# Optimization experiments

Measured on AMD Instinct MI355X. Metric: run time of the kernel, lower is better.

## Reference

```python
import jax, jax.numpy as jnp
import numpy as np

N = 100000
E = 800000
D = 128
THETA = (0.5, 0.3, 0.2)
NEG_SLOPE = 0.01  # torch F.leaky_relu default


def setup_inputs() -> dict:
    key = jax.random.key(0)
    ks = jax.random.split(key, 16)
    inv = 1.0 / np.sqrt(D)
    return {
        "src": jax.random.randint(ks[0], (E,), 0, N),
        "dst": jax.random.randint(ks[1], (E,), 0, N),
        "x0": jax.random.normal(ks[2], (N, D), jnp.float32),
        "x": jax.random.normal(ks[3], (N, D), jnp.float32),
        "e": jax.random.normal(ks[4], (N, D), jnp.float32),
        "labels": jax.random.randint(ks[5], (N,), 0, 2),
        "nid": jax.random.randint(ks[6], (N // 2,), 0, N),
        "alpha": jnp.full((1,), 0.5, jnp.float32),
        "emb": jax.random.normal(ks[7], (3, D), jnp.float32).at[2].set(0.0),  # padding_idx=2
        "pred_w1": jax.random.normal(ks[8], (D, D), jnp.float32) * inv,
        "pred_b1": jnp.zeros((D,), jnp.float32),
        "pred_w2": jax.random.normal(ks[9], (2, D), jnp.float32) * inv,
        "pred_b2": jnp.zeros((2,), jnp.float32),
        "weights": jax.random.uniform(ks[10], (2 * D, D), jnp.float32, -inv, inv),
        "lin_w": jax.random.normal(ks[11], (D, 2 * D), jnp.float32) * inv,
        "lin_b": jnp.zeros((D,), jnp.float32),
    }


def reference(src, dst, x0, x, e, labels, nid, alpha, emb,
              pred_w1, pred_b1, pred_w2, pred_b2, weights, lin_w, lin_b):
    # Predictor: MLP -> 2 logits, prob of class 1
    h = jax.nn.relu(x @ pred_w1.T + pred_b1)
    logits = h @ pred_w2.T + pred_b2                     # [N, 2]
    prob = jax.nn.softmax(logits, axis=1)[:, 1]          # [N]

    # NodeLabelEmbedding: soft mix of rows 0 and 1
    x_node = (1.0 - prob)[:, None] * emb[0] + prob[:, None] * emb[1]
    x_ = x
    xk = x + alpha * x_node

    # degree norm from edge list (in-degrees at dst)
    degs = jax.ops.segment_sum(jnp.ones_like(dst, dtype=xk.dtype), dst, num_segments=N)
    dinv = jnp.clip(degs, 1.0, None) ** -0.5             # [N]
    dinv = dinv[:, None]

    def unn_laplacian(feat):
        # feat - D^-1/2 A D^-1/2 feat  (messages src -> dst)
        msg = jax.ops.segment_sum((feat * dinv)[src], dst, num_segments=N)
        return feat - msg * dinv

    hi = THETA[0] * xk
    for k in range(1, len(THETA)):
        xk = unn_laplacian(xk)
        hi = hi + THETA[k] * xk

    hi = jnp.concatenate([hi, x_], axis=1)               # [N, 2D]
    outputs = hi @ weights                               # [N, D]
    out = jnp.concatenate([e, outputs], axis=1)          # [N, 2D]
    out = jax.nn.leaky_relu(out @ lin_w.T + lin_b, NEG_SLOPE)
    return out + x0                                      # residual
```

## Files before the change

kernel.cpp:

```cpp
#include <hip/hip_runtime.h>

#define N_NODES 100000
#define N_EDGES 800000
#define D 128

typedef __attribute__((ext_vector_type(8))) short short8;
typedef __attribute__((ext_vector_type(4))) float f32x4;

__device__ inline unsigned short f2bf(float f) {
  unsigned u = __float_as_uint(f);
  unsigned r = (u + 0x7fffu + ((u >> 16) & 1u)) >> 16;
  return (unsigned short)r;
}
__device__ inline void bfma8(float* acc, const uint4 v, float d) {
  acc[0] = fmaf(__uint_as_float(v.x << 16), d, acc[0]);
  acc[1] = fmaf(__uint_as_float(v.x & 0xffff0000u), d, acc[1]);
  acc[2] = fmaf(__uint_as_float(v.y << 16), d, acc[2]);
  acc[3] = fmaf(__uint_as_float(v.y & 0xffff0000u), d, acc[3]);
  acc[4] = fmaf(__uint_as_float(v.z << 16), d, acc[4]);
  acc[5] = fmaf(__uint_as_float(v.z & 0xffff0000u), d, acc[5]);
  acc[6] = fmaf(__uint_as_float(v.w << 16), d, acc[6]);
  acc[7] = fmaf(__uint_as_float(v.w & 0xffff0000u), d, acc[7]);
}
__device__ inline void unpack8(float* o, const uint4 v) {
  o[0] = __uint_as_float(v.x << 16); o[1] = __uint_as_float(v.x & 0xffff0000u);
  o[2] = __uint_as_float(v.y << 16); o[3] = __uint_as_float(v.y & 0xffff0000u);
  o[4] = __uint_as_float(v.z << 16); o[5] = __uint_as_float(v.z & 0xffff0000u);
  o[6] = __uint_as_float(v.w << 16); o[7] = __uint_as_float(v.w & 0xffff0000u);
}
__device__ inline uint4 pack8(const float* v) {
  uint4 r;
  r.x = (unsigned)f2bf(v[0]) | ((unsigned)f2bf(v[1]) << 16);
  r.y = (unsigned)f2bf(v[2]) | ((unsigned)f2bf(v[3]) << 16);
  r.z = (unsigned)f2bf(v[4]) | ((unsigned)f2bf(v[5]) << 16);
  r.w = (unsigned)f2bf(v[6]) | ((unsigned)f2bf(v[7]) << 16);
  return r;
}

__global__ void k_deg(const int* __restrict__ dst, int* __restrict__ degs) {
  int e = blockIdx.x * 256 + threadIdx.x;
  if (e < N_EDGES) atomicAdd(&degs[dst[e]], 1);
}

__global__ void k_scan1(const int* __restrict__ degs, int* __restrict__ offs,
                        int* __restrict__ aux) {
  __shared__ int s[256];
  int tid = threadIdx.x;
  int i = blockIdx.x * 256 + tid;
  int v = (i < N_NODES) ? degs[i] : 0;
  int sum = v;
  s[tid] = sum; __syncthreads();
  for (int off = 1; off < 256; off <<= 1) {
    int t = (tid >= off) ? s[tid - off] : 0;
    __syncthreads();
    sum += t; s[tid] = sum;
    __syncthreads();
  }
  if (i < N_NODES) offs[i] = sum - v;
  if (tid == 255) aux[blockIdx.x] = sum;
}

__global__ void k_scan2(const int* __restrict__ aux, int* __restrict__ aux2, int nblk) {
  __shared__ int s[512];
  int tid = threadIdx.x;
  int v = (tid < nblk) ? aux[tid] : 0;
  int sum = v;
  s[tid] = sum; __syncthreads();
  for (int off = 1; off < 512; off <<= 1) {
    int t = (tid >= off) ? s[tid - off] : 0;
    __syncthreads();
    sum += t; s[tid] = sum;
    __syncthreads();
  }
  aux2[tid] = sum - v;
}

__global__ void k_scan3(int* __restrict__ offs, const int* __restrict__ aux2,
                        const int* __restrict__ degs, float* __restrict__ dinv) {
  int i = blockIdx.x * 256 + threadIdx.x;
  if (i < N_NODES) {
    offs[i] += aux2[blockIdx.x];
    dinv[i] = rsqrtf(fmaxf((float)degs[i], 1.0f));
  }
}

__global__ void k_fill(const int* __restrict__ src, const int* __restrict__ dst,
                       const int* __restrict__ offs, int* __restrict__ cursor,
                       int* __restrict__ csr) {
  int e = blockIdx.x * 256 + threadIdx.x;
  if (e < N_EDGES) {
    int d = dst[e];
    int pos = offs[d] + atomicAdd(&cursor[d], 1);
    csr[pos] = src[e];
  }
}

__global__ __launch_bounds__(256, 2)
void k_mlp(const float* __restrict__ x, const float* __restrict__ w1,
           const float* __restrict__ w2, const float* __restrict__ b1,
           const float* __restrict__ b2, const float* __restrict__ emb,
           const float* __restrict__ alpha_p, unsigned short* __restrict__ xk_bf) {
  __shared__ __align__(16) float xsT[128 * 68];
  __shared__ __align__(16) float w1sT[32 * 128];
  __shared__ float zbuf[64];
  __shared__ float pbuf[64];

  int tid = threadIdx.x;
  int lane = tid & 63;
  int wave = tid >> 6;
  int n0 = blockIdx.x * 64;

  {
    int n = lane;
    int gn = n0 + n;
    const float4* xr = (const float4*)(x + (size_t)gn * 128 + wave * 32);
    #pragma unroll
    for (int i = 0; i < 8; i++) {
      float4 v = make_float4(0.f, 0.f, 0.f, 0.f);
      if (gn < N_NODES) v = xr[i];
      int k = wave * 32 + i * 4;
      xsT[(k + 0) * 68 + n] = v.x;
      xsT[(k + 1) * 68 + n] = v.y;
      xsT[(k + 2) * 68 + n] = v.z;
      xsT[(k + 3) * 68 + n] = v.w;
    }
  }

  int d8 = tid & 15;
  int n4 = tid >> 4;
  float acc[4][8];
  #pragma unroll
  for (int a = 0; a < 4; a++)
    #pragma unroll
    for (int c = 0; c < 8; c++) acc[a][c] = 0.f;

  for (int p = 0; p < 4; p++) {
    __syncthreads();
    {
      int j = tid >> 1;
      int kg0 = (tid & 1) * 4;
      const float4* wr = (const float4*)(w1 + j * 128 + p * 32);
      #pragma unroll
      for (int c = 0; c < 4; c++) {
        float4 v = wr[kg0 + c];
        int k = (kg0 + c) * 4;
        w1sT[(k + 0) * 128 + j] = v.x;
        w1sT[(k + 1) * 128 + j] = v.y;
        w1sT[(k + 2) * 128 + j] = v.z;
        w1sT[(k + 3) * 128 + j] = v.w;
      }
    }
    __syncthreads();

    for (int kk = 0; kk < 32; kk += 4) {
      float wq[4][8];
      float4 f[4];
      #pragma unroll
      for (int q = 0; q < 4; q++) {
        const float4* wr = (const float4*)(w1sT + (kk + q) * 128 + d8 * 8);
        float4 a = wr[0], b = wr[1];
        wq[q][0] = a.x; wq[q][1] = a.y; wq[q][2] = a.z; wq[q][3] = a.w;
        wq[q][4] = b.x; wq[q][5] = b.y; wq[q][6] = b.z; wq[q][7] = b.w;
        f[q] = *(const float4*)(xsT + (p * 32 + kk + q) * 68 + n4 * 4);
      }
      #pragma unroll
      for (int q = 0; q < 4; q++) {
        #pragma unroll
        for (int c = 0; c < 8; c++) {
          acc[0][c] += f[q].x * wq[q][c];
          acc[1][c] += f[q].y * wq[q][c];
          acc[2][c] += f[q].z * wq[q][c];
          acc[3][c] += f[q].w * wq[q][c];
        }
      }
    }
  }

  {
    int j0 = d8 * 8;
    float bb[8], wd[8];
    #pragma unroll
    for (int c = 0; c < 8; c++) {
      bb[c] = b1[j0 + c];
      wd[c] = w2[128 + j0 + c] - w2[j0 + c];
    }
    #pragma unroll
    for (int a = 0; a < 4; a++) {
      float s = 0.f;
      #pragma unroll
      for (int c = 0; c < 8; c++) {
        float h = fmaxf(acc[a][c] + bb[c], 0.f);
        s += h * wd[c];
      }
      s += __shfl_down(s, 8);
      s += __shfl_down(s, 4);
      s += __shfl_down(s, 2);
      s += __shfl_down(s, 1);
      if (d8 == 0) zbuf[n4 * 4 + a] = s;
    }
  }
  __syncthreads();
  if (tid < 64) {
    float db2 = b2[1] - b2[0];
    float z = zbuf[tid] + db2;
    pbuf[tid] = 1.f / (1.f + expf(-z));
  }
  __syncthreads();

  {
    float al = alpha_p[0];
    int d4 = tid & 31;
    const float4 e0 = ((const float4*)emb)[d4];
    const float4 e1 = ((const float4*)(emb + 128))[d4];
    #pragma unroll
    for (int i = 0; i < 8; i++) {
      int n = i * 8 + (tid >> 5);
      int gn = n0 + n;
      if (gn >= N_NODES) continue;
      float p = pbuf[n];
      float c0 = al * (1.f - p), c1 = al * p;
      float4 xv = ((const float4*)x)[(size_t)gn * 32 + d4];
      float o0 = xv.x + c0 * e0.x + c1 * e1.x;
      float o1 = xv.y + c0 * e0.y + c1 * e1.y;
      float o2 = xv.z + c0 * e0.z + c1 * e1.z;
      float o3 = xv.w + c0 * e0.w + c1 * e1.w;
      ushort4 ov = make_ushort4(f2bf(o0), f2bf(o1), f2bf(o2), f2bf(o3));
      ((ushort4*)xk_bf)[(size_t)gn * 32 + d4] = ov;
    }
  }
}

template <int PASS>
__global__ __launch_bounds__(256)
void k_gather(const unsigned short* __restrict__ feat,
              unsigned short* __restrict__ feat_out,
              float* __restrict__ hi,
              unsigned short* __restrict__ ahi,
              const int* __restrict__ csr, const int* __restrict__ offs,
              const int* __restrict__ degs, const float* __restrict__ dinv) {
  int node = blockIdx.x * 4 + (threadIdx.x >> 6);
  int lane = threadIdx.x & 63;
  int quad = lane >> 4;
  int l16 = lane & 15;
  int start = offs[node];
  int cnt = degs[node];
  const uint4* f16 = (const uint4*)feat;
  float acc[8];
  #pragma unroll
  for (int i = 0; i < 8; i++) acc[i] = 0.f;

  int j = 0;
  for (; j + 8 <= cnt; j += 8) {
    int sa = csr[start + j + quad];
    int sb = csr[start + j + 4 + quad];
    float da = dinv[sa], db = dinv[sb];
    uint4 va = f16[(size_t)sa * 16 + l16];
    uint4 vb = f16[(size_t)sb * 16 + l16];
    bfma8(acc, va, da);
    bfma8(acc, vb, db);
  }
  if (j + 4 <= cnt) {
    int s = csr[start + j + quad];
    float d = dinv[s];
    uint4 v = f16[(size_t)s * 16 + l16];
    bfma8(acc, v, d);
    j += 4;
  }
  int rem = cnt - j;
  if (quad < rem) {
    int s = csr[start + j + quad];
    float d = dinv[s];
    uint4 v = f16[(size_t)s * 16 + l16];
    bfma8(acc, v, d);
  }

  #pragma unroll
  for (int i = 0; i < 8; i++) {
    acc[i] += __shfl_down(acc[i], 32);
    acc[i] += __shfl_down(acc[i], 16);
  }

  if (quad == 0) {
    float dvi = dinv[node];
    float old[8], nw[8];
    unpack8(old, f16[(size_t)node * 16 + l16]);
    #pragma unroll
    for (int i = 0; i < 8; i++) nw[i] = old[i] - acc[i] * dvi;
    if (PASS == 1) {
      ((uint4*)feat_out)[(size_t)node * 16 + l16] = pack8(nw);
      float h[8];
      #pragma unroll
      for (int i = 0; i < 8; i++) h[i] = 0.5f * old[i] + 0.3f * nw[i];
      float4* hp = (float4*)(hi + (size_t)node * 128 + l16 * 8);
      hp[0] = make_float4(h[0], h[1], h[2], h[3]);
      hp[1] = make_float4(h[4], h[5], h[6], h[7]);
    } else {
      const float4* hp = (const float4*)(hi + (size_t)node * 128 + l16 * 8);
      float4 a = hp[0], b = hp[1];
      float h[8] = {a.x, a.y, a.z, a.w, b.x, b.y, b.z, b.w};
      #pragma unroll
      for (int i = 0; i < 8; i++) h[i] += 0.2f * nw[i];
      ((uint4*)ahi)[(size_t)node * 16 + l16] = pack8(h);
    }
  }
}

__global__ void k_pre(const float* __restrict__ weights, const float* __restrict__ lin_w,
                      unsigned short* __restrict__ wbt) {
  int gid = blockIdx.x * 256 + threadIdx.x;
  int k = gid >> 7, d = gid & 127;
  float v;
  if (k < 128) {
    v = lin_w[d * 256 + k];
  } else {
    const float* wrow = weights + (k - 128) * 128;
    const float* lcol = lin_w + d * 256 + 128;
    float s = 0.f;
    for (int j = 0; j < 128; j++) s += wrow[j] * lcol[j];
    v = s;
  }
  wbt[d * 392 + k] = f2bf(v);
}

__global__ __launch_bounds__(256, 2)
void k_gemm2(const float* __restrict__ ein, const unsigned short* __restrict__ ahi,
             const float* __restrict__ x, const unsigned short* __restrict__ wbt,
             const float* __restrict__ lin_b, const float* __restrict__ x0,
             float* __restrict__ out) {
  __shared__ __align__(16) unsigned short Bs[64 * 392];
  int tid = threadIdx.x;
  int lane = tid & 63, wv = tid >> 6;
  int quad = lane >> 4, l16 = lane & 15;
  int n0 = blockIdx.x * 64;
  int rA = n0 + wv * 16 + l16;
  if (rA >= N_NODES) rA = N_NODES - 1;
  int kq = quad * 8;

  short8 af[12];
  #pragma unroll
  for (int kb = 0; kb < 4; kb++) {
    const float4* p = (const float4*)(ein + (size_t)rA * 128 + kb * 32 + kq);
    float4 a = p[0], b = p[1];
    short8 t;
    t[0] = (short)f2bf(a.x); t[1] = (short)f2bf(a.y);
    t[2] = (short)f2bf(a.z); t[3] = (short)f2bf(a.w);
    t[4] = (short)f2bf(b.x); t[5] = (short)f2bf(b.y);
    t[6] = (short)f2bf(b.z); t[7] = (short)f2bf(b.w);
    af[kb] = t;
  }
  #pragma unroll
  for (int kb = 0; kb < 4; kb++)
    af[4 + kb] = *(const short8*)(ahi + (size_t)rA * 128 + kb * 32 + kq);
  #pragma unroll
  for (int kb = 0; kb < 4; kb++) {
    const float4* p = (const float4*)(x + (size_t)rA * 128 + kb * 32 + kq);
    float4 a = p[0], b = p[1];
    short8 t;
    t[0] = (short)f2bf(a.x); t[1] = (short)f2bf(a.y);
    t[2] = (short)f2bf(a.z); t[3] = (short)f2bf(a.w);
    t[4] = (short)f2bf(b.x); t[5] = (short)f2bf(b.y);
    t[6] = (short)f2bf(b.z); t[7] = (short)f2bf(b.w);
    af[8 + kb] = t;
  }

  f32x4 acc[8];
  #pragma unroll
  for (int i = 0; i < 8; i++) acc[i] = (f32x4){0.f, 0.f, 0.f, 0.f};

  for (int h = 0; h < 2; h++) {
    if (h) __syncthreads();
    {
      const uint4* W = (const uint4*)wbt;
      uint4* B4 = (uint4*)Bs;
      int r = tid >> 2, c0 = tid & 3;
      #pragma unroll
      for (int i = 0; i < 13; i++) {
        int c = c0 + i * 4;
        if (c < 49) B4[r * 49 + c] = W[(h * 64 + r) * 49 + c];
      }
    }
    __syncthreads();
    #pragma unroll
    for (int kb = 0; kb < 12; kb++) {
      short8 a = af[kb];
      #pragma unroll
      for (int t = 0; t < 4; t++) {
        short8 b = *(const short8*)(Bs + (t * 16 + l16) * 392 + kb * 32 + kq);
        acc[h * 4 + t] = __builtin_amdgcn_mfma_f32_16x16x32_bf16(a, b, acc[h * 4 + t], 0, 0, 0);
      }
    }
  }

  #pragma unroll
  for (int idx = 0; idx < 8; idx++) {
    int col = (idx >> 2) * 64 + (idx & 3) * 16 + l16;
    float bl = lin_b[col];
    #pragma unroll
    for (int r = 0; r < 4; r++) {
      int gn = n0 + wv * 16 + quad * 4 + r;
      if (gn < N_NODES) {
        float v = acc[idx][r] + bl;
        v = (v > 0.f) ? v : 0.01f * v;
        out[(size_t)gn * 128 + col] = v + x0[(size_t)gn * 128 + col];
      }
    }
  }
}

extern "C" void kernel_launch(void* const* d_in, const int* in_sizes, int n_in,
                              void* d_out, int out_size, void* d_ws, size_t ws_size,
                              hipStream_t stream) {
  const int*   src     = (const int*)d_in[0];
  const int*   dst     = (const int*)d_in[1];
  const float* x0      = (const float*)d_in[2];
  const float* x       = (const float*)d_in[3];
  const float* ein     = (const float*)d_in[4];
  const float* alpha   = (const float*)d_in[7];
  const float* emb     = (const float*)d_in[8];
  const float* w1      = (const float*)d_in[9];
  const float* b1      = (const float*)d_in[10];
  const float* w2      = (const float*)d_in[11];
  const float* b2      = (const float*)d_in[12];
  const float* weights = (const float*)d_in[13];
  const float* lin_w   = (const float*)d_in[14];
  const float* lin_b   = (const float*)d_in[15];
  float* out = (float*)d_out;

  unsigned short* xk_bf  = (unsigned short*)d_ws;
  unsigned short* xk1_bf = xk_bf  + (size_t)N_NODES * 128;
  unsigned short* ahi    = xk1_bf + (size_t)N_NODES * 128;
  unsigned short* wbt    = ahi    + (size_t)N_NODES * 128;
  float* dinv = (float*)(wbt + 128 * 392);
  int* degs   = (int*)(dinv + N_NODES);
  int* offs   = degs + N_NODES;
  int* cursor = offs + N_NODES;
  int* aux    = cursor + N_NODES;
  int* aux2   = aux + 512;
  int* csr    = aux2 + 512;

  hipMemsetAsync(degs, 0, sizeof(int) * 3 * (size_t)N_NODES, stream);

  int gE = (N_EDGES + 255) / 256;
  int gN = (N_NODES + 255) / 256;
  k_deg  <<<gE, 256, 0, stream>>>(dst, degs);
  k_scan1<<<gN, 256, 0, stream>>>(degs, offs, aux);
  k_scan2<<<1, 512, 0, stream>>>(aux, aux2, gN);
  k_scan3<<<gN, 256, 0, stream>>>(offs, aux2, degs, dinv);
  k_fill <<<gE, 256, 0, stream>>>(src, dst, offs, cursor, csr);

  k_mlp<<<(N_NODES + 63) / 64, 256, 0, stream>>>(x, w1, w2, b1, b2, emb, alpha, xk_bf);
  k_pre<<<192, 256, 0, stream>>>(weights, lin_w, wbt);

  float* hi = out;
  k_gather<1><<<N_NODES / 4, 256, 0, stream>>>(xk_bf,  xk1_bf, hi, nullptr, csr, offs, degs, dinv);
  k_gather<2><<<N_NODES / 4, 256, 0, stream>>>(xk1_bf, nullptr, hi, ahi,    csr, offs, degs, dinv);

  k_gemm2<<<(N_NODES + 63) / 64, 256, 0, stream>>>(ein, ahi, x, wbt, lin_b, x0, out);
}
```

Measured before the change: 492.1 us.

## Merge MLP, degree count and weight prep into one front kernel; shrink gemm2 LDS tile

Three independent kernels (the MLP, the in-degree atomic count and the weight precompute) become one launch that dispatches on block index, so they can overlap and two launches are saved. The final GEMM now stages B in four 32-column chunks instead of two 64-column ones, halving LDS so launch bounds can ask for 4 blocks per CU. The fused kernel's LDS footprint and register limit now apply to the simple degree and prep blocks too, and the GEMM adds more barriers and more chunk reloads.

```diff
diff --git a/kernel.cpp b/kernel.cpp
--- a/kernel.cpp
+++ b/kernel.cpp
@@ -3,6 +3,10 @@
 #define N_NODES 100000
 #define N_EDGES 800000
 #define D 128
+
+#define G_MLP 1563
+#define G_DEG 3125
+#define G_PRE 192
 
 typedef __attribute__((ext_vector_type(8))) short short8;
 typedef __attribute__((ext_vector_type(4))) float f32x4;
@@ -37,78 +41,47 @@
   return r;
 }
 
-__global__ void k_deg(const int* __restrict__ dst, int* __restrict__ degs) {
-  int e = blockIdx.x * 256 + threadIdx.x;
-  if (e < N_EDGES) atomicAdd(&degs[dst[e]], 1);
-}
-
-__global__ void k_scan1(const int* __restrict__ degs, int* __restrict__ offs,
-                        int* __restrict__ aux) {
-  __shared__ int s[256];
+__global__ __launch_bounds__(256, 2)
+void k_front(const float* __restrict__ x, const float* __restrict__ w1,
+             const float* __restrict__ w2, const float* __restrict__ b1,
+             const float* __restrict__ b2, const float* __restrict__ emb,
+             const float* __restrict__ alpha_p, unsigned short* __restrict__ xk_bf,
+             const int* __restrict__ dst, int* __restrict__ degs,
+             const float* __restrict__ weights, const float* __restrict__ lin_w,
+             unsigned short* __restrict__ wbt) {
   int tid = threadIdx.x;
-  int i = blockIdx.x * 256 + tid;
-  int v = (i < N_NODES) ? degs[i] : 0;
-  int sum = v;
-  s[tid] = sum; __syncthreads();
-  for (int off = 1; off < 256; off <<= 1) {
-    int t = (tid >= off) ? s[tid - off] : 0;
-    __syncthreads();
-    sum += t; s[tid] = sum;
-    __syncthreads();
-  }
-  if (i < N_NODES) offs[i] = sum - v;
-  if (tid == 255) aux[blockIdx.x] = sum;
-}
-
-__global__ void k_scan2(const int* __restrict__ aux, int* __restrict__ aux2, int nblk) {
-  __shared__ int s[512];
-  int tid = threadIdx.x;
-  int v = (tid < nblk) ? aux[tid] : 0;
-  int sum = v;
-  s[tid] = sum; __syncthreads();
-  for (int off = 1; off < 512; off <<= 1) {
-    int t = (tid >= off) ? s[tid - off] : 0;
-    __syncthreads();
-    sum += t; s[tid] = sum;
-    __syncthreads();
-  }
-  aux2[tid] = sum - v;
-}
-
-__global__ void k_scan3(int* __restrict__ offs, const int* __restrict__ aux2,
-                        const int* __restrict__ degs, float* __restrict__ dinv) {
-  int i = blockIdx.x * 256 + threadIdx.x;
-  if (i < N_NODES) {
-    offs[i] += aux2[blockIdx.x];
-    dinv[i] = rsqrtf(fmaxf((float)degs[i], 1.0f));
-  }
-}
-
-__global__ void k_fill(const int* __restrict__ src, const int* __restrict__ dst,
-                       const int* __restrict__ offs, int* __restrict__ cursor,
-                       int* __restrict__ csr) {
-  int e = blockIdx.x * 256 + threadIdx.x;
-  if (e < N_EDGES) {
-    int d = dst[e];
-    int pos = offs[d] + atomicAdd(&cursor[d], 1);
-    csr[pos] = src[e];
-  }
-}
-
-__global__ __launch_bounds__(256, 2)
-void k_mlp(const float* __restrict__ x, const float* __restrict__ w1,
-           const float* __restrict__ w2, const float* __restrict__ b1,
-           const float* __restrict__ b2, const float* __restrict__ emb,
-           const float* __restrict__ alpha_p, unsigned short* __restrict__ xk_bf) {
+  int bid = blockIdx.x;
+
+  if (bid >= G_MLP) {
+    if (bid < G_MLP + G_DEG) {
+      int e = (bid - G_MLP) * 256 + tid;
+      if (e < N_EDGES) atomicAdd(&degs[dst[e]], 1);
+    } else {
+      int gid = (bid - G_MLP - G_DEG) * 256 + tid;
+      int k = gid >> 7, d = gid & 127;
+      float v;
+      if (k < 128) {
+        v = lin_w[d * 256 + k];
+      } else {
+        const float* wrow = weights + (k - 128) * 128;
+        const float* lcol = lin_w + d * 256 + 128;
+        float s = 0.f;
+        for (int j = 0; j < 128; j++) s += wrow[j] * lcol[j];
+        v = s;
+      }
+      wbt[d * 392 + k] = f2bf(v);
+    }
+    return;
+  }
+
   __shared__ __align__(16) float xsT[128 * 68];
   __shared__ __align__(16) float w1sT[32 * 128];
   __shared__ float zbuf[64];
   __shared__ float pbuf[64];
 
-  int tid = threadIdx.x;
   int lane = tid & 63;
   int wave = tid >> 6;
-  int n0 = blockIdx.x * 64;
+  int n0 = bid * 64;
 
   {
     int n = lane;
@@ -227,6 +200,59 @@
       ushort4 ov = make_ushort4(f2bf(o0), f2bf(o1), f2bf(o2), f2bf(o3));
       ((ushort4*)xk_bf)[(size_t)gn * 32 + d4] = ov;
     }
+  }
+}
+
+__global__ void k_scan1(const int* __restrict__ degs, int* __restrict__ offs,
+                        int* __restrict__ aux) {
+  __shared__ int s[256];
+  int tid = threadIdx.x;
+  int i = blockIdx.x * 256 + tid;
+  int v = (i < N_NODES) ? degs[i] : 0;
+  int sum = v;
+  s[tid] = sum; __syncthreads();
+  for (int off = 1; off < 256; off <<= 1) {
+    int t = (tid >= off) ? s[tid - off] : 0;
+    __syncthreads();
+    sum += t; s[tid] = sum;
+    __syncthreads();
+  }
+  if (i < N_NODES) offs[i] = sum - v;
+  if (tid == 255) aux[blockIdx.x] = sum;
+}
+
+__global__ void k_scan2(const int* __restrict__ aux, int* __restrict__ aux2, int nblk) {
+  __shared__ int s[512];
+  int tid = threadIdx.x;
+  int v = (tid < nblk) ? aux[tid] : 0;
+  int sum = v;
+  s[tid] = sum; __syncthreads();
+  for (int off = 1; off < 512; off <<= 1) {
+    int t = (tid >= off) ? s[tid - off] : 0;
+    __syncthreads();
+    sum += t; s[tid] = sum;
+    __syncthreads();
+  }
+  aux2[tid] = sum - v;
+}
+
+__global__ void k_scan3(int* __restrict__ offs, const int* __restrict__ aux2,
+                        const int* __restrict__ degs, float* __restrict__ dinv) {
+  int i = blockIdx.x * 256 + threadIdx.x;
+  if (i < N_NODES) {
+    offs[i] += aux2[blockIdx.x];
+    dinv[i] = rsqrtf(fmaxf((float)degs[i], 1.0f));
+  }
+}
+
+__global__ void k_fill(const int* __restrict__ src, const int* __restrict__ dst,
+                       const int* __restrict__ offs, int* __restrict__ cursor,
+                       int* __restrict__ csr) {
+  int e = blockIdx.x * 256 + threadIdx.x;
+  if (e < N_EDGES) {
+    int d = dst[e];
+    int pos = offs[d] + atomicAdd(&cursor[d], 1);
+    csr[pos] = src[e];
   }
 }
 
@@ -305,29 +331,12 @@
   }
 }
 
-__global__ void k_pre(const float* __restrict__ weights, const float* __restrict__ lin_w,
-                      unsigned short* __restrict__ wbt) {
-  int gid = blockIdx.x * 256 + threadIdx.x;
-  int k = gid >> 7, d = gid & 127;
-  float v;
-  if (k < 128) {
-    v = lin_w[d * 256 + k];
-  } else {
-    const float* wrow = weights + (k - 128) * 128;
-    const float* lcol = lin_w + d * 256 + 128;
-    float s = 0.f;
-    for (int j = 0; j < 128; j++) s += wrow[j] * lcol[j];
-    v = s;
-  }
-  wbt[d * 392 + k] = f2bf(v);
-}
-
-__global__ __launch_bounds__(256, 2)
+__global__ __launch_bounds__(256, 4)
 void k_gemm2(const float* __restrict__ ein, const unsigned short* __restrict__ ahi,
              const float* __restrict__ x, const unsigned short* __restrict__ wbt,
              const float* __restrict__ lin_b, const float* __restrict__ x0,
              float* __restrict__ out) {
-  __shared__ __align__(16) unsigned short Bs[64 * 392];
+  __shared__ __align__(16) unsigned short Bs[32 * 392];
   int tid = threadIdx.x;
   int lane = tid & 63, wv = tid >> 6;
   int quad = lane >> 4, l16 = lane & 15;
@@ -367,16 +376,17 @@
   #pragma unroll
   for (int i = 0; i < 8; i++) acc[i] = (f32x4){0.f, 0.f, 0.f, 0.f};
 
-  for (int h = 0; h < 2; h++) {
-    if (h) __syncthreads();
+  #pragma unroll
+  for (int ch = 0; ch < 4; ch++) {
+    if (ch) __syncthreads();
     {
       const uint4* W = (const uint4*)wbt;
       uint4* B4 = (uint4*)Bs;
-      int r = tid >> 2, c0 = tid & 3;
-      #pragma unroll
-      for (int i = 0; i < 13; i++) {
-        int c = c0 + i * 4;
-        if (c < 49) B4[r * 49 + c] = W[(h * 64 + r) * 49 + c];
+      int r = tid >> 3, c0 = tid & 7;
+      #pragma unroll
+      for (int i = 0; i < 7; i++) {
+        int c = c0 + i * 8;
+        if (c < 49) B4[r * 49 + c] = W[(ch * 32 + r) * 49 + c];
       }
     }
     __syncthreads();
@@ -384,16 +394,16 @@
     for (int kb = 0; kb < 12; kb++) {
       short8 a = af[kb];
       #pragma unroll
-      for (int t = 0; t < 4; t++) {
+      for (int t = 0; t < 2; t++) {
         short8 b = *(const short8*)(Bs + (t * 16 + l16) * 392 + kb * 32 + kq);
-        acc[h * 4 + t] = __builtin_amdgcn_mfma_f32_16x16x32_bf16(a, b, acc[h * 4 + t], 0, 0, 0);
+        acc[ch * 2 + t] = __builtin_amdgcn_mfma_f32_16x16x32_bf16(a, b, acc[ch * 2 + t], 0, 0, 0);
       }
     }
   }
 
   #pragma unroll
   for (int idx = 0; idx < 8; idx++) {
-    int col = (idx >> 2) * 64 + (idx & 3) * 16 + l16;
+    int col = (idx >> 1) * 32 + (idx & 1) * 16 + l16;
     float bl = lin_b[col];
     #pragma unroll
     for (int r = 0; r < 4; r++) {
@@ -440,17 +450,17 @@
 
   hipMemsetAsync(degs, 0, sizeof(int) * 3 * (size_t)N_NODES, stream);
 
+  int gN = (N_NODES + 255) / 256;
   int gE = (N_EDGES + 255) / 256;
-  int gN = (N_NODES + 255) / 256;
-  k_deg  <<<gE, 256, 0, stream>>>(dst, degs);
+
+  k_front<<<G_MLP + G_DEG + G_PRE, 256, 0, stream>>>(
+      x, w1, w2, b1, b2, emb, alpha, xk_bf, dst, degs, weights, lin_w, wbt);
+
   k_scan1<<<gN, 256, 0, stream>>>(degs, offs, aux);
   k_scan2<<<1, 512, 0, stream>>>(aux, aux2, gN);
   k_scan3<<<gN, 256, 0, stream>>>(offs, aux2, degs, dinv);
   k_fill <<<gE, 256, 0, stream>>>(src, dst, offs, cursor, csr);
 
-  k_mlp<<<(N_NODES + 63) / 64, 256, 0, stream>>>(x, w1, w2, b1, b2, emb, alpha, xk_bf);
-  k_pre<<<192, 256, 0, stream>>>(weights, lin_w, wbt);
-
   float* hi = out;
   k_gather<1><<<N_NODES / 4, 256, 0, stream>>>(xk_bf,  xk1_bf, hi, nullptr, csr, offs, degs, dinv);
   k_gather<2><<<N_NODES / 4, 256, 0, stream>>>(xk1_bf, nullptr, hi, ahi,    csr, offs, degs, dinv);
```

New measurement: 465.1 us. -5.5%, faster.
